# Kernel optimization log

Measured on AMD Instinct MI355X. Metric: run time of the kernel, lower is better.

Reference implementation:

```python
import jax, jax.numpy as jnp
import numpy as np

B, S, E, NH = 2, 2048, 1024, 8
DH = E // NH


def setup_inputs() -> dict:
    key = jax.random.key(0)
    ks = jax.random.split(key, 8)
    q = jax.random.normal(ks[0], (B, S, E), dtype=jnp.float32)
    k = jax.random.normal(ks[1], (B, S, E), dtype=jnp.float32)
    v = jax.random.normal(ks[2], (B, S, E), dtype=jnp.float32)
    # gate projections: Linear(3E -> NH)
    igate_w = jax.random.normal(ks[3], (NH, 3 * E), dtype=jnp.float32) * 0.02
    igate_b = jax.random.normal(ks[4], (NH,), dtype=jnp.float32) * 0.1
    fgate_w = jax.random.normal(ks[5], (NH, 3 * E), dtype=jnp.float32) * 0.02
    fgate_b = jnp.linspace(3.0, 6.0, NH, dtype=jnp.float32)  # bias_linspace_init_
    norm_weight = 1.0 + 0.01 * jax.random.normal(ks[6], (E,), dtype=jnp.float32)
    return {"q": q, "k": k, "v": v, "igate_w": igate_w, "igate_b": igate_b,
            "fgate_w": fgate_w, "fgate_b": fgate_b, "norm_weight": norm_weight}


def _mlstm_forward(q, k, v, igate_w, igate_b, fgate_w, fgate_b, norm_weight):
    eps = 1e-6
    gate_in = jnp.concatenate([q, k, v], axis=-1)            # (B,S,3E)
    i_pre = gate_in @ igate_w.T + igate_b                    # (B,S,NH)
    f_pre = gate_in @ fgate_w.T + fgate_b                    # (B,S,NH)
    i_pre = jnp.transpose(i_pre, (0, 2, 1))                  # (B,NH,S)
    f_pre = jnp.transpose(f_pre, (0, 2, 1))                  # (B,NH,S)

    qh = jnp.transpose(q.reshape(B, S, NH, DH), (0, 2, 1, 3))  # (B,NH,S,DH)
    kh = jnp.transpose(k.reshape(B, S, NH, DH), (0, 2, 1, 3))
    vh = jnp.transpose(v.reshape(B, S, NH, DH), (0, 2, 1, 3))

    # cumulative log forget gates; decay matrix D[i,j] = sum_{u=j+1..i} logsig(f_u) + i_pre[j]
    log_fg = jax.nn.log_sigmoid(f_pre)                       # (B,NH,S)
    cs = jnp.cumsum(log_fg, axis=-1)                         # (B,NH,S)
    diff = cs[:, :, :, None] - cs[:, :, None, :]             # (B,NH,S,S) = cs[i]-cs[j]
    causal = jnp.tril(jnp.ones((S, S), dtype=bool))
    log_fg_mat = jnp.where(causal, diff, -jnp.inf)
    log_D = log_fg_mat + i_pre[:, :, None, :]                # (B,NH,S,S)

    max_log_D = jnp.max(log_D, axis=-1, keepdims=True)       # rowwise stabilizer
    D = jnp.exp(log_D - max_log_D)

    qk = jnp.einsum("bhsd,bhtd->bhst", qh, kh / jnp.sqrt(jnp.float32(DH)))
    C = qk * D
    normalizer = jnp.maximum(jnp.abs(jnp.sum(C, axis=-1, keepdims=True)),
                             jnp.exp(-max_log_D))
    Cn = C / (normalizer + eps)
    h = jnp.einsum("bhst,bhtd->bhsd", Cn, vh)                # (B,NH,S,DH)

    # MultiHeadLayerNorm == group_norm(num_groups=NH): per-head, per-token over DH
    mu = jnp.mean(h, axis=-1, keepdims=True)
    var = jnp.var(h, axis=-1, keepdims=True)
    hn = (h - mu) / jnp.sqrt(var + 1e-5)
    hn = hn * norm_weight.reshape(NH, DH)[None, :, None, :]
    return jnp.transpose(hn, (0, 2, 1, 3)).reshape(B, S, E)


def reference(q, k, v, igate_w, igate_b, fgate_w, fgate_b, norm_weight):
    return _mlstm_forward(q, k, v, igate_w, igate_b, fgate_w, fgate_b, norm_weight)
```

## Files before the change

### kernel.cpp

```cpp
#include <hip/hip_runtime.h>
#include <hip/hip_bf16.h>
#include <math.h>

typedef __attribute__((ext_vector_type(8))) short bf16x8;
typedef __attribute__((ext_vector_type(4))) float f32x4;

namespace {
constexpr int kB = 2, kS = 2048, kE = 1024, kNH = 8, kDH = 128, kE3 = 3072;
constexpr float kLog2e = 1.4426950408889634f;
constexpr int BM = 64, BN = 64;
constexpr int kHeavy = 16;
constexpr int kUnits = 16 + 2 * 16;
}

__device__ __forceinline__ ushort f2bf(float x) {
  union { __hip_bfloat16 b; ushort u; } c; c.b = __float2bfloat16(x); return c.u;
}
__device__ __forceinline__ uint pk2(float a, float b) {
  return (uint)f2bf(a) | ((uint)f2bf(b) << 16);
}
__device__ __forceinline__ void gload16(const void* g, void* l) {
  __builtin_amdgcn_global_load_lds(
      (const __attribute__((address_space(1))) void*)g,
      (__attribute__((address_space(3))) void*)l, 16, 0, 0);
}

__device__ __forceinline__ float butterfly64(float* acc, int lane) {
  int cur = 64;
#pragma unroll
  for (int lv = 0; lv < 6; ++lv) {
    const int bmask = 1 << lv;
    const int half = cur >> 1;
    const bool hi = (lane & bmask) != 0;
#pragma unroll
    for (int i = 0; i < 32; ++i) {
      if (i >= half) break;
      const float keep = hi ? acc[i + half] : acc[i];
      const float send = hi ? acc[i] : acc[i + half];
      acc[i] = keep + __shfl_xor(send, bmask);
    }
    cur = half;
  }
  return acc[0];
}

__global__ __launch_bounds__(256) void convkv_kernel(
    const float* __restrict__ k, const float* __restrict__ v,
    ushort* __restrict__ Kb, ushort* __restrict__ Vtb) {
  const int b = blockIdx.y;
  const int s0 = blockIdx.x * 8;
  const int tid = threadIdx.x;
  const int w = tid >> 6, lane = tid & 63;
  __shared__ ushort Vst[8 * 1024];

#pragma unroll
  for (int t = 0; t < 2; ++t) {
    const int tokl = w * 2 + t;
    const int s = s0 + tokl;
    const size_t base = ((size_t)b * kS + s) * kE + lane * 16;
    const float4 k0 = *reinterpret_cast<const float4*>(k + base);
    const float4 k1 = *reinterpret_cast<const float4*>(k + base + 4);
    const float4 k2 = *reinterpret_cast<const float4*>(k + base + 8);
    const float4 k3 = *reinterpret_cast<const float4*>(k + base + 12);
    uint4 pa, pb;
    pa.x = pk2(k0.x, k0.y); pa.y = pk2(k0.z, k0.w);
    pa.z = pk2(k1.x, k1.y); pa.w = pk2(k1.z, k1.w);
    pb.x = pk2(k2.x, k2.y); pb.y = pk2(k2.z, k2.w);
    pb.z = pk2(k3.x, k3.y); pb.w = pk2(k3.z, k3.w);
    ushort* kd = Kb + ((size_t)(b * 8 + (lane >> 3)) * kS + s) * 128 + (lane & 7) * 16;
    *reinterpret_cast<uint4*>(kd) = pa;
    *reinterpret_cast<uint4*>(kd + 8) = pb;

    const float4 v0 = *reinterpret_cast<const float4*>(v + base);
    const float4 v1 = *reinterpret_cast<const float4*>(v + base + 4);
    const float4 v2 = *reinterpret_cast<const float4*>(v + base + 8);
    const float4 v3 = *reinterpret_cast<const float4*>(v + base + 12);
    uint4 va, vb4;
    va.x = pk2(v0.x, v0.y); va.y = pk2(v0.z, v0.w);
    va.z = pk2(v1.x, v1.y); va.w = pk2(v1.z, v1.w);
    vb4.x = pk2(v2.x, v2.y); vb4.y = pk2(v2.z, v2.w);
    vb4.z = pk2(v3.x, v3.y); vb4.w = pk2(v3.z, v3.w);
    const int cc0 = lane * 2, cc1 = lane * 2 + 1;
    *reinterpret_cast<uint4*>(reinterpret_cast<char*>(Vst) + tokl * 2048 +
                              ((cc0 ^ ((cc0 >> 3) & 7)) << 4)) = va;
    *reinterpret_cast<uint4*>(reinterpret_cast<char*>(Vst) + tokl * 2048 +
                              ((cc1 ^ ((cc1 >> 3) & 7)) << 4)) = vb4;
  }
  __syncthreads();

#pragma unroll
  for (int j = 0; j < 4; ++j) {
    const int e = j * 256 + tid;
    const int cc = e >> 3;
    const int off = ((cc ^ ((cc >> 3) & 7)) << 4) + (e & 7) * 2;
    uint tmp[4];
#pragma unroll
    for (int t2 = 0; t2 < 8; t2 += 2) {
      const ushort u0 = *reinterpret_cast<const ushort*>(
          reinterpret_cast<const char*>(Vst) + t2 * 2048 + off);
      const ushort u1 = *reinterpret_cast<const ushort*>(
          reinterpret_cast<const char*>(Vst) + (t2 + 1) * 2048 + off);
      tmp[t2 >> 1] = (uint)u0 | ((uint)u1 << 16);
    }
    uint4 o; o.x = tmp[0]; o.y = tmp[1]; o.z = tmp[2]; o.w = tmp[3];
    ushort* vd = Vtb + ((size_t)(b * 8 + (e >> 7)) * 128 + (e & 127)) * kS + s0;
    *reinterpret_cast<uint4*>(vd) = o;
  }
}

__global__ __launch_bounds__(256) void gates_kernel(
    const float* __restrict__ q, const float* __restrict__ k, const float* __restrict__ v,
    const float* __restrict__ iw, const float* __restrict__ ib,
    const float* __restrict__ fw, const float* __restrict__ fb,
    float* __restrict__ i_pre, float* __restrict__ f_pre) {
  const int tid = threadIdx.x;
  const int w = tid >> 6, lane = tid & 63;
  const int tokbase = blockIdx.x * 8;
  const int kh = w >> 1, gh = w & 1;
  const float* __restrict__ W = gh ? fw : iw;

  float acc[64];
#pragma unroll
  for (int i = 0; i < 64; ++i) acc[i] = 0.f;

  for (int step = 0; step < 24; ++step) {
    const int e = kh * 1536 + step * 64 + lane;
    const int seg = e >> 10;
    const int eo = e & 1023;
    const float* __restrict__ src = (seg == 0) ? q : (seg == 1) ? k : v;
    float gv[8];
#pragma unroll
    for (int t = 0; t < 8; ++t)
      gv[t] = src[(size_t)(tokbase + t) * kE + eo];
    float w8[8];
#pragma unroll
    for (int hh = 0; hh < 8; ++hh) w8[hh] = W[hh * kE3 + e];
#pragma unroll
    for (int t = 0; t < 8; ++t)
#pragma unroll
      for (int hh = 0; hh < 8; ++hh)
        acc[t * 8 + hh] += gv[t] * w8[hh];
  }
  const float r = butterfly64(acc, lane);
  const int a = ((lane & 1) << 5) | ((lane & 2) << 3) | ((lane & 4) << 1) |
                ((lane & 8) >> 1) | ((lane & 16) >> 3) | ((lane & 32) >> 5);
  __shared__ float red[4][64];
  red[w][a] = r;
  __syncthreads();
  if (tid < 128) {
    const int t = tid >> 4, g16 = tid & 15, hh = g16 & 7;
    const float val = (g16 < 8) ? red[0][t * 8 + hh] + red[2][t * 8 + hh]
                                : red[1][t * 8 + hh] + red[3][t * 8 + hh];
    const int token = tokbase + t;
    const int b = token >> 11, s = token & 2047;
    const size_t idx = ((size_t)(b * 8 + hh)) * kS + s;
    if (g16 < 8) i_pre[idx] = val + ib[hh];
    else         f_pre[idx] = val + fb[hh];
  }
}

__global__ __launch_bounds__(256) void scan_kernel(
    const float* __restrict__ i_pre, const float* __restrict__ f_pre,
    float* __restrict__ a2_out, float* __restrict__ M2_out, float* __restrict__ nfl_out) {
  const int bh = blockIdx.x;
  const int tid = threadIdx.x;
  const int w = tid >> 6, lane = tid & 63;
  __shared__ float wsum[4], wmax[4];
  const float* __restrict__ fp = f_pre + (size_t)bh * kS;
  const float* __restrict__ ip = i_pre + (size_t)bh * kS;
  const int s0 = tid * 8;

  const float4 fa = *reinterpret_cast<const float4*>(fp + s0);
  const float4 fb4 = *reinterpret_cast<const float4*>(fp + s0 + 4);
  float lf[8];
  {
    const float fv[8] = {fa.x, fa.y, fa.z, fa.w, fb4.x, fb4.y, fb4.z, fb4.w};
#pragma unroll
    for (int j = 0; j < 8; ++j)
      lf[j] = fminf(fv[j], 0.f) - log1pf(expf(-fabsf(fv[j])));
  }
  float run = 0.f, pcs[8];
#pragma unroll
  for (int j = 0; j < 8; ++j) { run += lf[j]; pcs[j] = run; }
  float x = run;
#pragma unroll
  for (int d = 1; d < 64; d <<= 1) {
    const float t = __shfl_up(x, d);
    if (lane >= d) x += t;
  }
  if (lane == 63) wsum[w] = x;
  __syncthreads();
  float woff = 0.f;
#pragma unroll
  for (int i = 0; i < 4; ++i) if (i < w) woff += wsum[i];
  const float csbase = woff + x - run;
  float cs[8];
#pragma unroll
  for (int j = 0; j < 8; ++j) cs[j] = csbase + pcs[j];

  const float4 ia = *reinterpret_cast<const float4*>(ip + s0);
  const float4 ib4 = *reinterpret_cast<const float4*>(ip + s0 + 4);
  float av[8];
  {
    const float iv[8] = {ia.x, ia.y, ia.z, ia.w, ib4.x, ib4.y, ib4.z, ib4.w};
#pragma unroll
    for (int j = 0; j < 8; ++j) av[j] = iv[j] - cs[j];
  }
  float rmax = -1e30f, pm[8];
#pragma unroll
  for (int j = 0; j < 8; ++j) { rmax = fmaxf(rmax, av[j]); pm[j] = rmax; }
  float mi = rmax;
#pragma unroll
  for (int d = 1; d < 64; d <<= 1) {
    const float t = __shfl_up(mi, d);
    if (lane >= d) mi = fmaxf(mi, t);
  }
  if (lane == 63) wmax[w] = mi;
  float mexcl = __shfl_up(mi, 1);
  if (lane == 0) mexcl = -1e30f;
  __syncthreads();
  float wmoff = -1e30f;
#pragma unroll
  for (int i = 0; i < 4; ++i) if (i < w) wmoff = fmaxf(wmoff, wmax[i]);
  const float mbase = fmaxf(wmoff, mexcl);

  float M[8];
#pragma unroll
  for (int j = 0; j < 8; ++j) M[j] = fmaxf(mbase, pm[j]);
  float4 a2lo, a2hi, m2lo, m2hi, nflo, nfhi;
  a2lo.x = av[0] * kLog2e; a2lo.y = av[1] * kLog2e; a2lo.z = av[2] * kLog2e; a2lo.w = av[3] * kLog2e;
  a2hi.x = av[4] * kLog2e; a2hi.y = av[5] * kLog2e; a2hi.z = av[6] * kLog2e; a2hi.w = av[7] * kLog2e;
  m2lo.x = M[0] * kLog2e; m2lo.y = M[1] * kLog2e; m2lo.z = M[2] * kLog2e; m2lo.w = M[3] * kLog2e;
  m2hi.x = M[4] * kLog2e; m2hi.y = M[5] * kLog2e; m2hi.z = M[6] * kLog2e; m2hi.w = M[7] * kLog2e;
  nflo.x = expf(-(cs[0] + M[0])); nflo.y = expf(-(cs[1] + M[1]));
  nflo.z = expf(-(cs[2] + M[2])); nflo.w = expf(-(cs[3] + M[3]));
  nfhi.x = expf(-(cs[4] + M[4])); nfhi.y = expf(-(cs[5] + M[5]));
  nfhi.z = expf(-(cs[6] + M[6])); nfhi.w = expf(-(cs[7] + M[7]));
  const size_t o = (size_t)bh * kS + s0;
  *reinterpret_cast<float4*>(a2_out + o) = a2lo;
  *reinterpret_cast<float4*>(a2_out + o + 4) = a2hi;
  *reinterpret_cast<float4*>(M2_out + o) = m2lo;
  *reinterpret_cast<float4*>(M2_out + o + 4) = m2hi;
  *reinterpret_cast<float4*>(nfl_out + o) = nflo;
  *reinterpret_cast<float4*>(nfl_out + o + 4) = nfhi;
}

__device__ __forceinline__ void epilogue_store(
    f32x4* hacc, float rsum, float nf, int b, int h, int srow, int g,
    const float* __restrict__ nw, float* __restrict__ out) {
  const float inv = 1.f / (fmaxf(fabsf(rsum), nf) + 1e-6f);
  float ps = 0.f, pq = 0.f;
#pragma unroll
  for (int db = 0; db < 8; ++db) {
#pragma unroll
    for (int reg = 0; reg < 4; ++reg) {
      const float hv = hacc[db][reg] * inv;
      hacc[db][reg] = hv;
      ps += hv; pq += hv * hv;
    }
  }
  ps += __shfl_xor(ps, 16); ps += __shfl_xor(ps, 32);
  pq += __shfl_xor(pq, 16); pq += __shfl_xor(pq, 32);
  const float mu = ps * (1.f / 128.f);
  const float var = pq * (1.f / 128.f) - mu * mu;
  const float rstd = rsqrtf(var + 1e-5f);
  float* __restrict__ orow = out + ((size_t)b * kS + srow) * kE + h * kDH;
#pragma unroll
  for (int db = 0; db < 8; ++db) {
    const int d0 = db * 16 + g * 4;
    const float4 nw4 = *reinterpret_cast<const float4*>(nw + h * kDH + d0);
    float4 o;
    o.x = (hacc[db][0] - mu) * rstd * nw4.x;
    o.y = (hacc[db][1] - mu) * rstd * nw4.y;
    o.z = (hacc[db][2] - mu) * rstd * nw4.z;
    o.w = (hacc[db][3] - mu) * rstd * nw4.w;
    *reinterpret_cast<float4*>(orow + d0) = o;
  }
}

__global__ __launch_bounds__(256, 2) void attn_mfma_kernel(
    const float* __restrict__ qg, const ushort* __restrict__ Kb,
    const ushort* __restrict__ Vtb,
    const float* __restrict__ a2, const float* __restrict__ M2,
    const float* __restrict__ nfl, const float* __restrict__ nw,
    float* __restrict__ out, float* __restrict__ ph, float* __restrict__ prs) {
  const int bh = blockIdx.y;
  const int b = bh >> 3, h = bh & 7;
  const int u = kUnits - 1 - (int)blockIdx.x;
  int it, j0, j1, chunk = -1;
  if (u < kHeavy) { it = u; j0 = 0; j1 = it; }
  else {
    const int t = (u - kHeavy) >> 1, c = (u - kHeavy) & 1;
    it = kHeavy + t;
    const int m = (it + 1) >> 1;
    if (c == 0) { j0 = 0; j1 = m - 1; } else { j0 = m; j1 = it; }
    chunk = ((bh * 16) + t) * 2 + c;
  }
  const int tid = threadIdx.x;
  const int w = tid >> 6, lane = tid & 63;
  const int l15 = lane & 15, g = lane >> 4;
  const int row0 = it * BM;
  const int rowbase = row0 + w * 16;
  const size_t bhS = (size_t)bh * kS;

  __shared__ ushort Klds[2 * BN * kDH];
  __shared__ ushort Vlds[2 * kDH * BN];
  __shared__ ushort Plds[4][16 * BN];

  const char* __restrict__ KgBase = reinterpret_cast<const char*>(Kb + bhS * 128);
  const char* __restrict__ VgBase = reinterpret_cast<const char*>(Vtb + (size_t)bh * 128 * kS);

  bf16x8 qf[4];
  {
    const float scale = 0.08838834764831845f;
    const float* qrow = qg + ((size_t)b * kS + rowbase + l15) * kE + h * kDH;
#pragma unroll
    for (int ks = 0; ks < 4; ++ks) {
      const float4 lo = *reinterpret_cast<const float4*>(qrow + ks * 32 + g * 8);
      const float4 hi = *reinterpret_cast<const float4*>(qrow + ks * 32 + g * 8 + 4);
      bf16x8 f;
      f[0] = (short)f2bf(lo.x * scale); f[1] = (short)f2bf(lo.y * scale);
      f[2] = (short)f2bf(lo.z * scale); f[3] = (short)f2bf(lo.w * scale);
      f[4] = (short)f2bf(hi.x * scale); f[5] = (short)f2bf(hi.y * scale);
      f[6] = (short)f2bf(hi.z * scale); f[7] = (short)f2bf(hi.w * scale);
      qf[ks] = f;
    }
  }
  float M2row[4];
#pragma unroll
  for (int reg = 0; reg < 4; ++reg) M2row[reg] = M2[bhS + rowbase + g * 4 + reg];

  int koffG[4], voffG[4];
#pragma unroll
  for (int i = 0; i < 4; ++i) {
    const int L = tid * 16 + i * 4096;
    { const int j = L >> 8, c = (L >> 4) & 15;
      koffG[i] = j * 256 + ((c ^ (j & 7)) << 4); }
    { const int d = L >> 7, c = (L >> 4) & 7;
      voffG[i] = d * 4096 + ((c ^ (d & 7)) << 4); }
  }

  auto stage = [&](int buf, int jt) {
    const char* Kg = KgBase + (size_t)jt * 16384;
    const char* Vg = VgBase + (size_t)jt * 128;
    char* kl = reinterpret_cast<char*>(Klds) + buf * 16384 + tid * 16;
    char* vl = reinterpret_cast<char*>(Vlds) + buf * 16384 + tid * 16;
#pragma unroll
    for (int i = 0; i < 4; ++i) gload16(Kg + koffG[i], kl + i * 4096);
#pragma unroll
    for (int i = 0; i < 4; ++i) gload16(Vg + voffG[i], vl + i * 4096);
  };

  f32x4 hacc[8];
#pragma unroll
  for (int db = 0; db < 8; ++db) hacc[db] = (f32x4){0.f, 0.f, 0.f, 0.f};
  float rs[4] = {0.f, 0.f, 0.f, 0.f};

  float avc[4];
#pragma unroll
  for (int cb = 0; cb < 4; ++cb) avc[cb] = a2[bhS + j0 * 64 + cb * 16 + l15];
  stage(0, j0);
  __syncthreads();

  for (int jt = j0; jt <= j1; ++jt) {
    const int cur = (jt - j0) & 1;
    float avn[4];
    if (jt < j1) {
      stage(cur ^ 1, jt + 1);
#pragma unroll
      for (int cb = 0; cb < 4; ++cb)
        avn[cb] = a2[bhS + (jt + 1) * 64 + cb * 16 + l15];
    }

    const int kbase = cur * 16384;
    f32x4 sacc[4];
#pragma unroll
    for (int cb = 0; cb < 4; ++cb) sacc[cb] = (f32x4){0.f, 0.f, 0.f, 0.f};
#pragma unroll
    for (int ks = 0; ks < 4; ++ks) {
#pragma unroll
      for (int cb = 0; cb < 4; ++cb) {
        const int j = cb * 16 + l15;
        const int kb = kbase + j * 256 + ((ks * 64 + g * 16) ^ ((l15 & 7) << 4));
        const bf16x8 kf = *reinterpret_cast<const bf16x8*>(
            reinterpret_cast<const char*>(Klds) + kb);
        sacc[cb] = __builtin_amdgcn_mfma_f32_16x16x32_bf16(qf[ks], kf, sacc[cb], 0, 0, 0);
      }
    }

#pragma unroll
    for (int cb = 0; cb < 4; ++cb) {
      const int jg = jt * 64 + cb * 16 + l15;
#pragma unroll
      for (int reg = 0; reg < 4; ++reg) {
        const int ig = rowbase + g * 4 + reg;
        float val = 0.f;
        if (jg <= ig) val = sacc[cb][reg] * exp2f(avc[cb] - M2row[reg]);
        rs[reg] += val;
        const int r = g * 4 + reg;
        const int pb = r * 128 + ((cb * 32 + l15 * 2) ^ ((r & 7) << 4));
        *reinterpret_cast<ushort*>(
            reinterpret_cast<char*>(&Plds[w][0]) + pb) = f2bf(val);
      }
    }

    const int vbase = cur * 16384;
#pragma unroll
    for (int ks2 = 0; ks2 < 2; ++ks2) {
      const int pbyte = l15 * 128 + ((ks2 * 64 + g * 16) ^ ((l15 & 7) << 4));
      const bf16x8 pf = *reinterpret_cast<const bf16x8*>(
          reinterpret_cast<const char*>(&Plds[w][0]) + pbyte);
#pragma unroll
      for (int db = 0; db < 8; ++db) {
        const int d = db * 16 + l15;
        const int vb = vbase + d * 128 + ((ks2 * 64 + g * 16) ^ ((d & 7) << 4));
        const bf16x8 vf = *reinterpret_cast<const bf16x8*>(
            reinterpret_cast<const char*>(Vlds) + vb);
        hacc[db] = __builtin_amdgcn_mfma_f32_16x16x32_bf16(vf, pf, hacc[db], 0, 0, 0);
      }
    }
    __syncthreads();
    if (jt < j1) {
#pragma unroll
      for (int cb = 0; cb < 4; ++cb) avc[cb] = avn[cb];
    }
  }

#pragma unroll
  for (int reg = 0; reg < 4; ++reg) {
    float x = rs[reg];
    x += __shfl_xor(x, 1); x += __shfl_xor(x, 2);
    x += __shfl_xor(x, 4); x += __shfl_xor(x, 8);
    rs[reg] = x;
  }

  if (chunk >= 0) {
    float* pdst = ph + (size_t)chunk * (BM * kDH) + tid * 32;
#pragma unroll
    for (int db = 0; db < 8; ++db)
      *reinterpret_cast<float4*>(pdst + db * 4) =
          make_float4(hacc[db][0], hacc[db][1], hacc[db][2], hacc[db][3]);
    if (l15 == 0) {
#pragma unroll
      for (int reg = 0; reg < 4; ++reg)
        prs[chunk * BM + w * 16 + g * 4 + reg] = rs[reg];
    }
    return;
  }

  float* rsp = reinterpret_cast<float*>(&Plds[w][0]);
  if (l15 == 0) {
#pragma unroll
    for (int reg = 0; reg < 4; ++reg) rsp[g * 4 + reg] = rs[reg];
  }
  const float rsum = rsp[l15];
  const float nf = nfl[bhS + rowbase + l15];
  epilogue_store(hacc, rsum, nf, b, h, rowbase + l15, g, nw, out);
}

__global__ __launch_bounds__(256) void combine_kernel(
    const float* __restrict__ ph, const float* __restrict__ prs,
    const float* __restrict__ nfl, const float* __restrict__ nw,
    float* __restrict__ out) {
  const int blk = blockIdx.x;
  const int bh = blk >> 4, t = blk & 15;
  const int b = bh >> 3, h = bh & 7;
  const int it = kHeavy + t;
  const int tid = threadIdx.x;
  const int w = tid >> 6, lane = tid & 63;
  const int l15 = lane & 15, g = lane >> 4;
  const int rowbase = it * BM + w * 16;
  const int c0 = blk * 2, c1 = blk * 2 + 1;

  f32x4 hacc[8];
  const float* p0 = ph + (size_t)c0 * (BM * kDH) + tid * 32;
  const float* p1 = ph + (size_t)c1 * (BM * kDH) + tid * 32;
#pragma unroll
  for (int db = 0; db < 8; ++db) {
    const float4 a = *reinterpret_cast<const float4*>(p0 + db * 4);
    const float4 c = *reinterpret_cast<const float4*>(p1 + db * 4);
    hacc[db] = (f32x4){a.x + c.x, a.y + c.y, a.z + c.z, a.w + c.w};
  }
  const float rsum = prs[c0 * BM + w * 16 + l15] + prs[c1 * BM + w * 16 + l15];
  const float nf = nfl[(size_t)bh * kS + rowbase + l15];
  epilogue_store(hacc, rsum, nf, b, h, rowbase + l15, g, nw, out);
}

extern "C" void kernel_launch(void* const* d_in, const int* in_sizes, int n_in,
                              void* d_out, int out_size, void* d_ws, size_t ws_size,
                              hipStream_t stream) {
  const float* q  = (const float*)d_in[0];
  const float* k  = (const float*)d_in[1];
  const float* v  = (const float*)d_in[2];
  const float* iw = (const float*)d_in[3];
  const float* ib = (const float*)d_in[4];
  const float* fw = (const float*)d_in[5];
  const float* fb = (const float*)d_in[6];
  const float* nw = (const float*)d_in[7];
  float* out = (float*)d_out;

  char* ws = (char*)d_ws;
  const int BHS = kB * kNH * kS;
  float* i_pre = (float*)ws;
  float* f_pre = i_pre + BHS;
  float* a2    = i_pre + 2 * BHS;
  float* M2    = i_pre + 3 * BHS;
  float* nfl   = i_pre + 4 * BHS;
  char* ws2 = ws + (size_t)5 * BHS * 4;
  ushort* Kb  = (ushort*)ws2;
  ushort* Vtb = Kb + (size_t)kB * kNH * kS * kDH;
  float* ph   = (float*)(Vtb + (size_t)kB * kNH * kS * kDH);
  float* prs  = ph + (size_t)512 * BM * kDH;

  convkv_kernel<<<dim3(kS / 8, kB), dim3(256), 0, stream>>>(k, v, Kb, Vtb);
  gates_kernel<<<dim3(kB * kS / 8), dim3(256), 0, stream>>>(q, k, v, iw, ib, fw, fb,
                                                            i_pre, f_pre);
  scan_kernel<<<dim3(kB * kNH), dim3(256), 0, stream>>>(i_pre, f_pre, a2, M2, nfl);
  attn_mfma_kernel<<<dim3(kUnits, kB * kNH), dim3(256), 0, stream>>>(
      q, Kb, Vtb, a2, M2, nfl, nw, out, ph, prs);
  combine_kernel<<<dim3(kB * kNH * 16), dim3(256), 0, stream>>>(ph, prs, nfl, nw, out);
}
```

Measured before the change: 122.4 us.

## Factor decay weights per key block and switch attention to 32x32 MFMA tiles

The scan now emits per-key weights exp(a - blockmax) plus a per-64-key-block maximum, so the attention kernel forms the decay as a per-tile scalar times a per-column weight instead of taking an exponential per element. The attention kernel moves to 128-row query tiles with 32x32x16 bf16 MFMA, 64-key tiles, and a new hand-tuned order of 27 work units that split the heavy query tiles into 2 or 3 chunks. The combine kernel is generalized to sum a variable number of partials, and convkv is moved after the scan. Factoring the exponential can underflow or lose precision when the row max and block max are far apart, and the larger register tiles may lower occupancy.

New measurement: 118.4 us. 1.03x faster.

```diff
diff --git a/kernel.cpp b/kernel.cpp
--- a/kernel.cpp
+++ b/kernel.cpp
@@ -3,15 +3,17 @@
 #include <math.h>
 
 typedef __attribute__((ext_vector_type(8))) short bf16x8;
-typedef __attribute__((ext_vector_type(4))) float f32x4;
+typedef __attribute__((ext_vector_type(16))) float f32x16;
 
 namespace {
 constexpr int kB = 2, kS = 2048, kE = 1024, kNH = 8, kDH = 128, kE3 = 3072;
 constexpr float kLog2e = 1.4426950408889634f;
-constexpr int BM = 64, BN = 64;
-constexpr int kHeavy = 16;
-constexpr int kUnits = 16 + 2 * 16;
-}
+constexpr int kUnits = 27;
+constexpr int kSplitPerBh = 20;
+}
+
+__device__ const int kOrder[kUnits] = {6,19,20,17,18,5,15,16,13,14,24,25,4,
+                                       11,12,21,22,23,26,9,10,3,7,8,2,1,0};
 
 __device__ __forceinline__ ushort f2bf(float x) {
   union { __hip_bfloat16 b; ushort u; } c; c.b = __float2bfloat16(x); return c.u;
@@ -24,6 +26,13 @@
       (const __attribute__((address_space(1))) void*)g,
       (__attribute__((address_space(3))) void*)l, 16, 0, 0);
 }
+__device__ __forceinline__ f32x16 zero16() {
+  f32x16 z;
+#pragma unroll
+  for (int i = 0; i < 16; ++i) z[i] = 0.f;
+  return z;
+}
+union UB8 { uint4 u; bf16x8 f; };
 
 __device__ __forceinline__ float butterfly64(float* acc, int lane) {
   int cur = 64;
@@ -42,70 +51,6 @@
     cur = half;
   }
   return acc[0];
-}
-
-__global__ __launch_bounds__(256) void convkv_kernel(
-    const float* __restrict__ k, const float* __restrict__ v,
-    ushort* __restrict__ Kb, ushort* __restrict__ Vtb) {
-  const int b = blockIdx.y;
-  const int s0 = blockIdx.x * 8;
-  const int tid = threadIdx.x;
-  const int w = tid >> 6, lane = tid & 63;
-  __shared__ ushort Vst[8 * 1024];
-
-#pragma unroll
-  for (int t = 0; t < 2; ++t) {
-    const int tokl = w * 2 + t;
-    const int s = s0 + tokl;
-    const size_t base = ((size_t)b * kS + s) * kE + lane * 16;
-    const float4 k0 = *reinterpret_cast<const float4*>(k + base);
-    const float4 k1 = *reinterpret_cast<const float4*>(k + base + 4);
-    const float4 k2 = *reinterpret_cast<const float4*>(k + base + 8);
-    const float4 k3 = *reinterpret_cast<const float4*>(k + base + 12);
-    uint4 pa, pb;
-    pa.x = pk2(k0.x, k0.y); pa.y = pk2(k0.z, k0.w);
-    pa.z = pk2(k1.x, k1.y); pa.w = pk2(k1.z, k1.w);
-    pb.x = pk2(k2.x, k2.y); pb.y = pk2(k2.z, k2.w);
-    pb.z = pk2(k3.x, k3.y); pb.w = pk2(k3.z, k3.w);
-    ushort* kd = Kb + ((size_t)(b * 8 + (lane >> 3)) * kS + s) * 128 + (lane & 7) * 16;
-    *reinterpret_cast<uint4*>(kd) = pa;
-    *reinterpret_cast<uint4*>(kd + 8) = pb;
-
-    const float4 v0 = *reinterpret_cast<const float4*>(v + base);
-    const float4 v1 = *reinterpret_cast<const float4*>(v + base + 4);
-    const float4 v2 = *reinterpret_cast<const float4*>(v + base + 8);
-    const float4 v3 = *reinterpret_cast<const float4*>(v + base + 12);
-    uint4 va, vb4;
-    va.x = pk2(v0.x, v0.y); va.y = pk2(v0.z, v0.w);
-    va.z = pk2(v1.x, v1.y); va.w = pk2(v1.z, v1.w);
-    vb4.x = pk2(v2.x, v2.y); vb4.y = pk2(v2.z, v2.w);
-    vb4.z = pk2(v3.x, v3.y); vb4.w = pk2(v3.z, v3.w);
-    const int cc0 = lane * 2, cc1 = lane * 2 + 1;
-    *reinterpret_cast<uint4*>(reinterpret_cast<char*>(Vst) + tokl * 2048 +
-                              ((cc0 ^ ((cc0 >> 3) & 7)) << 4)) = va;
-    *reinterpret_cast<uint4*>(reinterpret_cast<char*>(Vst) + tokl * 2048 +
-                              ((cc1 ^ ((cc1 >> 3) & 7)) << 4)) = vb4;
-  }
-  __syncthreads();
-
-#pragma unroll
-  for (int j = 0; j < 4; ++j) {
-    const int e = j * 256 + tid;
-    const int cc = e >> 3;
-    const int off = ((cc ^ ((cc >> 3) & 7)) << 4) + (e & 7) * 2;
-    uint tmp[4];
-#pragma unroll
-    for (int t2 = 0; t2 < 8; t2 += 2) {
-      const ushort u0 = *reinterpret_cast<const ushort*>(
-          reinterpret_cast<const char*>(Vst) + t2 * 2048 + off);
-      const ushort u1 = *reinterpret_cast<const ushort*>(
-          reinterpret_cast<const char*>(Vst) + (t2 + 1) * 2048 + off);
-      tmp[t2 >> 1] = (uint)u0 | ((uint)u1 << 16);
-    }
-    uint4 o; o.x = tmp[0]; o.y = tmp[1]; o.z = tmp[2]; o.w = tmp[3];
-    ushort* vd = Vtb + ((size_t)(b * 8 + (e >> 7)) * 128 + (e & 127)) * kS + s0;
-    *reinterpret_cast<uint4*>(vd) = o;
-  }
 }
 
 __global__ __launch_bounds__(256) void gates_kernel(
@@ -161,7 +106,8 @@
 
 __global__ __launch_bounds__(256) void scan_kernel(
     const float* __restrict__ i_pre, const float* __restrict__ f_pre,
-    float* __restrict__ a2_out, float* __restrict__ M2_out, float* __restrict__ nfl_out) {
+    float* __restrict__ wt_out, float* __restrict__ M2_out, float* __restrict__ nfl_out,
+    float* __restrict__ Cg) {
   const int bh = blockIdx.x;
   const int tid = threadIdx.x;
   const int w = tid >> 6, lane = tid & 63;
@@ -209,6 +155,19 @@
   float rmax = -1e30f, pm[8];
 #pragma unroll
   for (int j = 0; j < 8; ++j) { rmax = fmaxf(rmax, av[j]); pm[j] = rmax; }
+
+  float tm = rmax;
+  tm = fmaxf(tm, __shfl_xor(tm, 1));
+  tm = fmaxf(tm, __shfl_xor(tm, 2));
+  tm = fmaxf(tm, __shfl_xor(tm, 4));
+  if ((lane & 7) == 0) Cg[bh * 32 + (tid >> 3)] = tm * kLog2e;
+
+  float4 wtlo, wthi;
+  wtlo.x = exp2f((av[0] - tm) * kLog2e); wtlo.y = exp2f((av[1] - tm) * kLog2e);
+  wtlo.z = exp2f((av[2] - tm) * kLog2e); wtlo.w = exp2f((av[3] - tm) * kLog2e);
+  wthi.x = exp2f((av[4] - tm) * kLog2e); wthi.y = exp2f((av[5] - tm) * kLog2e);
+  wthi.z = exp2f((av[6] - tm) * kLog2e); wthi.w = exp2f((av[7] - tm) * kLog2e);
+
   float mi = rmax;
 #pragma unroll
   for (int d = 1; d < 64; d <<= 1) {
@@ -227,9 +186,7 @@
   float M[8];
 #pragma unroll
   for (int j = 0; j < 8; ++j) M[j] = fmaxf(mbase, pm[j]);
-  float4 a2lo, a2hi, m2lo, m2hi, nflo, nfhi;
-  a2lo.x = av[0] * kLog2e; a2lo.y = av[1] * kLog2e; a2lo.z = av[2] * kLog2e; a2lo.w = av[3] * kLog2e;
-  a2hi.x = av[4] * kLog2e; a2hi.y = av[5] * kLog2e; a2hi.z = av[6] * kLog2e; a2hi.w = av[7] * kLog2e;
+  float4 m2lo, m2hi, nflo, nfhi;
   m2lo.x = M[0] * kLog2e; m2lo.y = M[1] * kLog2e; m2lo.z = M[2] * kLog2e; m2lo.w = M[3] * kLog2e;
   m2hi.x = M[4] * kLog2e; m2hi.y = M[5] * kLog2e; m2hi.z = M[6] * kLog2e; m2hi.w = M[7] * kLog2e;
   nflo.x = expf(-(cs[0] + M[0])); nflo.y = expf(-(cs[1] + M[1]));
@@ -237,109 +194,146 @@
   nfhi.x = expf(-(cs[4] + M[4])); nfhi.y = expf(-(cs[5] + M[5]));
   nfhi.z = expf(-(cs[6] + M[6])); nfhi.w = expf(-(cs[7] + M[7]));
   const size_t o = (size_t)bh * kS + s0;
-  *reinterpret_cast<float4*>(a2_out + o) = a2lo;
-  *reinterpret_cast<float4*>(a2_out + o + 4) = a2hi;
+  *reinterpret_cast<float4*>(wt_out + o) = wtlo;
+  *reinterpret_cast<float4*>(wt_out + o + 4) = wthi;
   *reinterpret_cast<float4*>(M2_out + o) = m2lo;
   *reinterpret_cast<float4*>(M2_out + o + 4) = m2hi;
   *reinterpret_cast<float4*>(nfl_out + o) = nflo;
   *reinterpret_cast<float4*>(nfl_out + o + 4) = nfhi;
 }
 
-__device__ __forceinline__ void epilogue_store(
-    f32x4* hacc, float rsum, float nf, int b, int h, int srow, int g,
-    const float* __restrict__ nw, float* __restrict__ out) {
-  const float inv = 1.f / (fmaxf(fabsf(rsum), nf) + 1e-6f);
-  float ps = 0.f, pq = 0.f;
-#pragma unroll
-  for (int db = 0; db < 8; ++db) {
-#pragma unroll
-    for (int reg = 0; reg < 4; ++reg) {
-      const float hv = hacc[db][reg] * inv;
-      hacc[db][reg] = hv;
-      ps += hv; pq += hv * hv;
-    }
-  }
-  ps += __shfl_xor(ps, 16); ps += __shfl_xor(ps, 32);
-  pq += __shfl_xor(pq, 16); pq += __shfl_xor(pq, 32);
-  const float mu = ps * (1.f / 128.f);
-  const float var = pq * (1.f / 128.f) - mu * mu;
-  const float rstd = rsqrtf(var + 1e-5f);
-  float* __restrict__ orow = out + ((size_t)b * kS + srow) * kE + h * kDH;
-#pragma unroll
-  for (int db = 0; db < 8; ++db) {
-    const int d0 = db * 16 + g * 4;
-    const float4 nw4 = *reinterpret_cast<const float4*>(nw + h * kDH + d0);
-    float4 o;
-    o.x = (hacc[db][0] - mu) * rstd * nw4.x;
-    o.y = (hacc[db][1] - mu) * rstd * nw4.y;
-    o.z = (hacc[db][2] - mu) * rstd * nw4.z;
-    o.w = (hacc[db][3] - mu) * rstd * nw4.w;
-    *reinterpret_cast<float4*>(orow + d0) = o;
+__global__ __launch_bounds__(256) void convkv_kernel(
+    const float* __restrict__ k, const float* __restrict__ v,
+    ushort* __restrict__ Kb, ushort* __restrict__ Vtb) {
+  const int b = blockIdx.y;
+  const int s0 = blockIdx.x * 8;
+  const int tid = threadIdx.x;
+  const int w = tid >> 6, lane = tid & 63;
+  __shared__ ushort Vst[8 * 1024];
+
+#pragma unroll
+  for (int t = 0; t < 2; ++t) {
+    const int tokl = w * 2 + t;
+    const int s = s0 + tokl;
+    const size_t base = ((size_t)b * kS + s) * kE + lane * 16;
+    const int hh = lane >> 3;
+
+    const float4 k0 = *reinterpret_cast<const float4*>(k + base);
+    const float4 k1 = *reinterpret_cast<const float4*>(k + base + 4);
+    const float4 k2 = *reinterpret_cast<const float4*>(k + base + 8);
+    const float4 k3 = *reinterpret_cast<const float4*>(k + base + 12);
+    uint4 pa, pb;
+    pa.x = pk2(k0.x, k0.y); pa.y = pk2(k0.z, k0.w);
+    pa.z = pk2(k1.x, k1.y); pa.w = pk2(k1.z, k1.w);
+    pb.x = pk2(k2.x, k2.y); pb.y = pk2(k2.z, k2.w);
+    pb.z = pk2(k3.x, k3.y); pb.w = pk2(k3.z, k3.w);
+    ushort* kd = Kb + ((size_t)(b * 8 + hh) * kS + s) * 128 + (lane & 7) * 16;
+    *reinterpret_cast<uint4*>(kd) = pa;
+    *reinterpret_cast<uint4*>(kd + 8) = pb;
+
+    const float4 v0 = *reinterpret_cast<const float4*>(v + base);
+    const float4 v1 = *reinterpret_cast<const float4*>(v + base + 4);
+    const float4 v2 = *reinterpret_cast<const float4*>(v + base + 8);
+    const float4 v3 = *reinterpret_cast<const float4*>(v + base + 12);
+    uint4 va, vb4;
+    va.x = pk2(v0.x, v0.y); va.y = pk2(v0.z, v0.w);
+    va.z = pk2(v1.x, v1.y); va.w = pk2(v1.z, v1.w);
+    vb4.x = pk2(v2.x, v2.y); vb4.y = pk2(v2.z, v2.w);
+    vb4.z = pk2(v3.x, v3.y); vb4.w = pk2(v3.z, v3.w);
+    const int cc0 = lane * 2, cc1 = lane * 2 + 1;
+    *reinterpret_cast<uint4*>(reinterpret_cast<char*>(Vst) + tokl * 2048 +
+                              ((cc0 ^ ((cc0 >> 3) & 7)) << 4)) = va;
+    *reinterpret_cast<uint4*>(reinterpret_cast<char*>(Vst) + tokl * 2048 +
+                              ((cc1 ^ ((cc1 >> 3) & 7)) << 4)) = vb4;
+  }
+  __syncthreads();
+
+#pragma unroll
+  for (int j = 0; j < 4; ++j) {
+    const int e = j * 256 + tid;
+    const int cc = e >> 3;
+    const int off = ((cc ^ ((cc >> 3) & 7)) << 4) + (e & 7) * 2;
+    uint tmp[4];
+#pragma unroll
+    for (int t2 = 0; t2 < 8; t2 += 2) {
+      const ushort u0 = *reinterpret_cast<const ushort*>(
+          reinterpret_cast<const char*>(Vst) + t2 * 2048 + off);
+      const ushort u1 = *reinterpret_cast<const ushort*>(
+          reinterpret_cast<const char*>(Vst) + (t2 + 1) * 2048 + off);
+      tmp[t2 >> 1] = (uint)u0 | ((uint)u1 << 16);
+    }
+    uint4 o; o.x = tmp[0]; o.y = tmp[1]; o.z = tmp[2]; o.w = tmp[3];
+    ushort* vd = Vtb + ((size_t)(b * 8 + (e >> 7)) * 128 + (e & 127)) * kS + s0;
+    *reinterpret_cast<uint4*>(vd) = o;
   }
 }
 
 __global__ __launch_bounds__(256, 2) void attn_mfma_kernel(
     const float* __restrict__ qg, const ushort* __restrict__ Kb,
-    const ushort* __restrict__ Vtb,
-    const float* __restrict__ a2, const float* __restrict__ M2,
+    const ushort* __restrict__ Vtb, const float* __restrict__ wt,
+    const float* __restrict__ Cg, const float* __restrict__ M2,
     const float* __restrict__ nfl, const float* __restrict__ nw,
     float* __restrict__ out, float* __restrict__ ph, float* __restrict__ prs) {
   const int bh = blockIdx.y;
   const int b = bh >> 3, h = bh & 7;
-  const int u = kUnits - 1 - (int)blockIdx.x;
-  int it, j0, j1, chunk = -1;
-  if (u < kHeavy) { it = u; j0 = 0; j1 = it; }
-  else {
-    const int t = (u - kHeavy) >> 1, c = (u - kHeavy) & 1;
-    it = kHeavy + t;
-    const int m = (it + 1) >> 1;
-    if (c == 0) { j0 = 0; j1 = m - 1; } else { j0 = m; j1 = it; }
-    chunk = ((bh * 16) + t) * 2 + c;
+  const int u = kOrder[blockIdx.x];
+  int it, j0, j1, cid = -1;
+  if (u <= 6) { it = u; const int T = 2 * it + 2; j0 = 0; j1 = T - 1; }
+  else if (u <= 20) {
+    const int s = u - 7; it = 7 + (s >> 1); const int ci = s & 1;
+    const int T = 2 * it + 2;
+    j0 = (T * ci) >> 1; j1 = ((T * (ci + 1)) >> 1) - 1;
+    cid = bh * kSplitPerBh + (u - 7);
+  } else {
+    const int s = u - 21; it = 14 + (s >= 3 ? 1 : 0); const int ci = s - (s >= 3 ? 3 : 0);
+    const int T = 2 * it + 2;
+    j0 = (T * ci) / 3; j1 = (T * (ci + 1)) / 3 - 1;
+    cid = bh * kSplitPerBh + (u - 7);
   }
   const int tid = threadIdx.x;
   const int w = tid >> 6, lane = tid & 63;
-  const int l15 = lane & 15, g = lane >> 4;
-  const int row0 = it * BM;
-  const int rowbase = row0 + w * 16;
+  const int l31 = lane & 31, hi = lane >> 5;
+  const int row_w = it * 128 + w * 32;
+  const int ig = row_w + l31;
   const size_t bhS = (size_t)bh * kS;
 
-  __shared__ ushort Klds[2 * BN * kDH];
-  __shared__ ushort Vlds[2 * kDH * BN];
-  __shared__ ushort Plds[4][16 * BN];
+  __shared__ ushort Klds[2 * 64 * 128];
+  __shared__ ushort Vlds[2 * 128 * 64];
+  __shared__ float Wlds[2 * 64];
+  __shared__ float rsx[4][32];
 
   const char* __restrict__ KgBase = reinterpret_cast<const char*>(Kb + bhS * 128);
   const char* __restrict__ VgBase = reinterpret_cast<const char*>(Vtb + (size_t)bh * 128 * kS);
-
-  bf16x8 qf[4];
+  const char* __restrict__ WgBase = reinterpret_cast<const char*>(wt + bhS);
+
+  bf16x8 qf[8];
   {
     const float scale = 0.08838834764831845f;
-    const float* qrow = qg + ((size_t)b * kS + rowbase + l15) * kE + h * kDH;
-#pragma unroll
-    for (int ks = 0; ks < 4; ++ks) {
-      const float4 lo = *reinterpret_cast<const float4*>(qrow + ks * 32 + g * 8);
-      const float4 hi = *reinterpret_cast<const float4*>(qrow + ks * 32 + g * 8 + 4);
-      bf16x8 f;
-      f[0] = (short)f2bf(lo.x * scale); f[1] = (short)f2bf(lo.y * scale);
-      f[2] = (short)f2bf(lo.z * scale); f[3] = (short)f2bf(lo.w * scale);
-      f[4] = (short)f2bf(hi.x * scale); f[5] = (short)f2bf(hi.y * scale);
-      f[6] = (short)f2bf(hi.z * scale); f[7] = (short)f2bf(hi.w * scale);
-      qf[ks] = f;
-    }
-  }
-  float M2row[4];
-#pragma unroll
-  for (int reg = 0; reg < 4; ++reg) M2row[reg] = M2[bhS + rowbase + g * 4 + reg];
+    const float* qrow = qg + ((size_t)b * kS + ig) * kE + h * kDH;
+#pragma unroll
+    for (int ks = 0; ks < 8; ++ks) {
+      const int d0 = ks * 16 + hi * 8;
+      const float4 lo = *reinterpret_cast<const float4*>(qrow + d0);
+      const float4 hi4 = *reinterpret_cast<const float4*>(qrow + d0 + 4);
+      UB8 f;
+      f.u.x = pk2(lo.x * scale, lo.y * scale);
+      f.u.y = pk2(lo.z * scale, lo.w * scale);
+      f.u.z = pk2(hi4.x * scale, hi4.y * scale);
+      f.u.w = pk2(hi4.z * scale, hi4.w * scale);
+      qf[ks] = f.f;
+    }
+  }
+  const float M2i = M2[bhS + ig];
 
   int koffG[4], voffG[4];
 #pragma unroll
   for (int i = 0; i < 4; ++i) {
     const int L = tid * 16 + i * 4096;
     { const int j = L >> 8, c = (L >> 4) & 15;
-      koffG[i] = j * 256 + ((c ^ (j & 7)) << 4); }
+      koffG[i] = j * 256 + ((c ^ (j & 15)) << 4); }
     { const int d = L >> 7, c = (L >> 4) & 7;
       voffG[i] = d * 4096 + ((c ^ (d & 7)) << 4); }
   }
-
   auto stage = [&](int buf, int jt) {
     const char* Kg = KgBase + (size_t)jt * 16384;
     const char* Vg = VgBase + (size_t)jt * 128;
@@ -349,113 +343,133 @@
     for (int i = 0; i < 4; ++i) gload16(Kg + koffG[i], kl + i * 4096);
 #pragma unroll
     for (int i = 0; i < 4; ++i) gload16(Vg + voffG[i], vl + i * 4096);
+    if (tid < 16)
+      gload16(WgBase + jt * 256 + tid * 16,
+              reinterpret_cast<char*>(Wlds) + buf * 256 + tid * 16);
   };
 
-  f32x4 hacc[8];
-#pragma unroll
-  for (int db = 0; db < 8; ++db) hacc[db] = (f32x4){0.f, 0.f, 0.f, 0.f};
-  float rs[4] = {0.f, 0.f, 0.f, 0.f};
-
-  float avc[4];
-#pragma unroll
-  for (int cb = 0; cb < 4; ++cb) avc[cb] = a2[bhS + j0 * 64 + cb * 16 + l15];
+  f32x16 hacc[4];
+#pragma unroll
+  for (int dc = 0; dc < 4; ++dc) hacc[dc] = zero16();
+  float rs = 0.f;
+
   stage(0, j0);
   __syncthreads();
 
   for (int jt = j0; jt <= j1; ++jt) {
     const int cur = (jt - j0) & 1;
-    float avn[4];
-    if (jt < j1) {
-      stage(cur ^ 1, jt + 1);
-#pragma unroll
-      for (int cb = 0; cb < 4; ++cb)
-        avn[cb] = a2[bhS + (jt + 1) * 64 + cb * 16 + l15];
-    }
-
-    const int kbase = cur * 16384;
-    f32x4 sacc[4];
-#pragma unroll
-    for (int cb = 0; cb < 4; ++cb) sacc[cb] = (f32x4){0.f, 0.f, 0.f, 0.f};
-#pragma unroll
-    for (int ks = 0; ks < 4; ++ks) {
-#pragma unroll
-      for (int cb = 0; cb < 4; ++cb) {
-        const int j = cb * 16 + l15;
-        const int kb = kbase + j * 256 + ((ks * 64 + g * 16) ^ ((l15 & 7) << 4));
-        const bf16x8 kf = *reinterpret_cast<const bf16x8*>(
-            reinterpret_cast<const char*>(Klds) + kb);
-        sacc[cb] = __builtin_amdgcn_mfma_f32_16x16x32_bf16(qf[ks], kf, sacc[cb], 0, 0, 0);
+    if (jt < j1) stage(cur ^ 1, jt + 1);
+    const int jlo = jt * 64;
+    const bool v0 = (jlo <= row_w + 31);
+    const bool v1 = (jlo + 32 <= row_w + 31);
+    const bool fullmask = (jlo + 63 <= row_w);
+
+    if (v0) {
+      const float f = exp2f(Cg[bh * 32 + jt] - M2i);
+      const char* kb = reinterpret_cast<const char*>(Klds) + cur * 16384;
+      const char* vb = reinterpret_cast<const char*>(Vlds) + cur * 16384;
+      const float* Wf = Wlds + cur * 64;
+      const int ksw = (l31 & 15) << 4;
+
+      f32x16 sacc0 = zero16(), sacc1 = zero16();
+#pragma unroll
+      for (int ks = 0; ks < 8; ++ks) {
+        const int colb = 32 * ks + 16 * hi;
+        const bf16x8 kf0 = *reinterpret_cast<const bf16x8*>(
+            kb + l31 * 256 + (colb ^ ksw));
+        sacc0 = __builtin_amdgcn_mfma_f32_32x32x16_bf16(kf0, qf[ks], sacc0, 0, 0, 0);
+        if (v1) {
+          const bf16x8 kf1 = *reinterpret_cast<const bf16x8*>(
+              kb + (32 + l31) * 256 + (colb ^ ksw));
+          sacc1 = __builtin_amdgcn_mfma_f32_32x32x16_bf16(kf1, qf[ks], sacc1, 0, 0, 0);
+        }
       }
-    }
-
-#pragma unroll
-    for (int cb = 0; cb < 4; ++cb) {
-      const int jg = jt * 64 + cb * 16 + l15;
-#pragma unroll
-      for (int reg = 0; reg < 4; ++reg) {
-        const int ig = rowbase + g * 4 + reg;
-        float val = 0.f;
-        if (jg <= ig) val = sacc[cb][reg] * exp2f(avc[cb] - M2row[reg]);
-        rs[reg] += val;
-        const int r = g * 4 + reg;
-        const int pb = r * 128 + ((cb * 32 + l15 * 2) ^ ((r & 7) << 4));
-        *reinterpret_cast<ushort*>(
-            reinterpret_cast<char*>(&Plds[w][0]) + pb) = f2bf(val);
+
+      uint pkw[2][8];
+#pragma unroll
+      for (int jc = 0; jc < 2; ++jc) {
+        if (jc == 1 && !v1) break;
+        const f32x16 sa = jc ? sacc1 : sacc0;
+        float p[16];
+#pragma unroll
+        for (int r = 0; r < 16; ++r) {
+          const int joff = jc * 32 + (r & 3) + 8 * (r >> 2) + 4 * hi;
+          float val = sa[r] * (Wf[joff] * f);
+          if (!fullmask) val = (jlo + joff <= ig) ? val : 0.f;
+          rs += val; p[r] = val;
+        }
+#pragma unroll
+        for (int q2 = 0; q2 < 8; ++q2) pkw[jc][q2] = pk2(p[2 * q2], p[2 * q2 + 1]);
       }
-    }
-
-    const int vbase = cur * 16384;
-#pragma unroll
-    for (int ks2 = 0; ks2 < 2; ++ks2) {
-      const int pbyte = l15 * 128 + ((ks2 * 64 + g * 16) ^ ((l15 & 7) << 4));
-      const bf16x8 pf = *reinterpret_cast<const bf16x8*>(
-          reinterpret_cast<const char*>(&Plds[w][0]) + pbyte);
-#pragma unroll
-      for (int db = 0; db < 8; ++db) {
-        const int d = db * 16 + l15;
-        const int vb = vbase + d * 128 + ((ks2 * 64 + g * 16) ^ ((d & 7) << 4));
-        const bf16x8 vf = *reinterpret_cast<const bf16x8*>(
-            reinterpret_cast<const char*>(Vlds) + vb);
-        hacc[db] = __builtin_amdgcn_mfma_f32_16x16x32_bf16(vf, pf, hacc[db], 0, 0, 0);
+
+#pragma unroll
+      for (int ks = 0; ks < 4; ++ks) {
+        const int jc = ks >> 1, ks2 = ks & 1;
+        if (jc == 1 && !v1) break;
+        UB8 pf;
+        pf.u.x = pkw[jc][ks2 * 4 + 0]; pf.u.y = pkw[jc][ks2 * 4 + 1];
+        pf.u.z = pkw[jc][ks2 * 4 + 2]; pf.u.w = pkw[jc][ks2 * 4 + 3];
+        const int colb = 64 * jc + 32 * ks2 + 8 * hi;
+#pragma unroll
+        for (int dc = 0; dc < 4; ++dc) {
+          const int d = dc * 32 + l31;
+          const char* vrow = vb + d * 128;
+          const int sw = (d & 7) << 4;
+          const uint2 a = *reinterpret_cast<const uint2*>(vrow + (colb ^ sw));
+          const uint2 c = *reinterpret_cast<const uint2*>(vrow + ((colb + 16) ^ sw));
+          UB8 vf; vf.u.x = a.x; vf.u.y = a.y; vf.u.z = c.x; vf.u.w = c.y;
+          hacc[dc] = __builtin_amdgcn_mfma_f32_32x32x16_bf16(pf.f, vf.f, hacc[dc], 0, 0, 0);
+        }
       }
     }
     __syncthreads();
-    if (jt < j1) {
-#pragma unroll
-      for (int cb = 0; cb < 4; ++cb) avc[cb] = avn[cb];
-    }
-  }
-
-#pragma unroll
-  for (int reg = 0; reg < 4; ++reg) {
-    float x = rs[reg];
-    x += __shfl_xor(x, 1); x += __shfl_xor(x, 2);
-    x += __shfl_xor(x, 4); x += __shfl_xor(x, 8);
-    rs[reg] = x;
-  }
-
-  if (chunk >= 0) {
-    float* pdst = ph + (size_t)chunk * (BM * kDH) + tid * 32;
-#pragma unroll
-    for (int db = 0; db < 8; ++db)
-      *reinterpret_cast<float4*>(pdst + db * 4) =
-          make_float4(hacc[db][0], hacc[db][1], hacc[db][2], hacc[db][3]);
-    if (l15 == 0) {
-#pragma unroll
-      for (int reg = 0; reg < 4; ++reg)
-        prs[chunk * BM + w * 16 + g * 4 + reg] = rs[reg];
-    }
+  }
+
+  const float rs_tot = rs + __shfl_xor(rs, 32);
+
+  if (cid >= 0) {
+    float* pb = ph + (size_t)cid * 16384;
+#pragma unroll
+    for (int dc = 0; dc < 4; ++dc)
+#pragma unroll
+      for (int r = 0; r < 16; ++r) {
+        const int il = w * 32 + (r & 3) + 8 * (r >> 2) + 4 * hi;
+        pb[il * 128 + dc * 32 + l31] = hacc[dc][r];
+      }
+    if (hi == 0) prs[cid * 128 + w * 32 + l31] = rs_tot;
     return;
   }
 
-  float* rsp = reinterpret_cast<float*>(&Plds[w][0]);
-  if (l15 == 0) {
-#pragma unroll
-    for (int reg = 0; reg < 4; ++reg) rsp[g * 4 + reg] = rs[reg];
-  }
-  const float rsum = rsp[l15];
-  const float nf = nfl[bhS + rowbase + l15];
-  epilogue_store(hacc, rsum, nf, b, h, rowbase + l15, g, nw, out);
+  if (hi == 0) rsx[w][l31] = rs_tot;
+  float nwv[4];
+#pragma unroll
+  for (int dc = 0; dc < 4; ++dc) nwv[dc] = nw[h * kDH + dc * 32 + l31];
+#pragma unroll
+  for (int r = 0; r < 16; ++r) {
+    const int imap = (r & 3) + 8 * (r >> 2) + 4 * hi;
+    const float rsum = rsx[w][imap];
+    const float nf = nfl[bhS + row_w + imap];
+    const float inv = 1.f / (fmaxf(fabsf(rsum), nf) + 1e-6f);
+    float hv[4];
+    float s1 = 0.f, s2 = 0.f;
+#pragma unroll
+    for (int dc = 0; dc < 4; ++dc) {
+      hv[dc] = hacc[dc][r] * inv;
+      s1 += hv[dc]; s2 += hv[dc] * hv[dc];
+    }
+#pragma unroll
+    for (int off = 1; off <= 16; off <<= 1) {
+      s1 += __shfl_xor(s1, off);
+      s2 += __shfl_xor(s2, off);
+    }
+    const float mu = s1 * (1.f / 128.f);
+    const float var = s2 * (1.f / 128.f) - mu * mu;
+    const float rstd = rsqrtf(var + 1e-5f);
+    float* __restrict__ orow = out + ((size_t)b * kS + row_w + imap) * kE + h * kDH;
+#pragma unroll
+    for (int dc = 0; dc < 4; ++dc)
+      orow[dc * 32 + l31] = (hv[dc] - mu) * rstd * nwv[dc];
+  }
 }
 
 __global__ __launch_bounds__(256) void combine_kernel(
@@ -463,27 +477,50 @@
     const float* __restrict__ nfl, const float* __restrict__ nw,
     float* __restrict__ out) {
   const int blk = blockIdx.x;
-  const int bh = blk >> 4, t = blk & 15;
+  const int bh = blk / 9, ct = blk % 9;
   const int b = bh >> 3, h = bh & 7;
-  const int it = kHeavy + t;
+  const int it = 7 + ct;
+  const int nc = (ct < 7) ? 2 : 3;
+  const int cb0 = bh * kSplitPerBh + ((ct < 7) ? ct * 2 : 14 + (ct - 7) * 3);
   const int tid = threadIdx.x;
-  const int w = tid >> 6, lane = tid & 63;
-  const int l15 = lane & 15, g = lane >> 4;
-  const int rowbase = it * BM + w * 16;
-  const int c0 = blk * 2, c1 = blk * 2 + 1;
-
-  f32x4 hacc[8];
-  const float* p0 = ph + (size_t)c0 * (BM * kDH) + tid * 32;
-  const float* p1 = ph + (size_t)c1 * (BM * kDH) + tid * 32;
-#pragma unroll
-  for (int db = 0; db < 8; ++db) {
-    const float4 a = *reinterpret_cast<const float4*>(p0 + db * 4);
-    const float4 c = *reinterpret_cast<const float4*>(p1 + db * 4);
-    hacc[db] = (f32x4){a.x + c.x, a.y + c.y, a.z + c.z, a.w + c.w};
-  }
-  const float rsum = prs[c0 * BM + w * 16 + l15] + prs[c1 * BM + w * 16 + l15];
-  const float nf = nfl[(size_t)bh * kS + rowbase + l15];
-  epilogue_store(hacc, rsum, nf, b, h, rowbase + l15, g, nw, out);
+  __shared__ float sinv[128];
+  if (tid < 128) {
+    float rsum = 0.f;
+    for (int c = 0; c < nc; ++c) rsum += prs[(cb0 + c) * 128 + tid];
+    const float nf = nfl[(size_t)bh * kS + it * 128 + tid];
+    sinv[tid] = 1.f / (fmaxf(fabsf(rsum), nf) + 1e-6f);
+  }
+  __syncthreads();
+  for (int kk = 0; kk < 16; ++kk) {
+    const int idx = kk * 256 + tid;
+    const int row = idx >> 5, c4 = idx & 31;
+    float ax = 0.f, ay = 0.f, az = 0.f, aw = 0.f;
+    for (int c = 0; c < nc; ++c) {
+      const float4 t = *reinterpret_cast<const float4*>(
+          ph + (size_t)(cb0 + c) * 16384 + row * 128 + c4 * 4);
+      ax += t.x; ay += t.y; az += t.z; aw += t.w;
+    }
+    const float inv = sinv[row];
+    ax *= inv; ay *= inv; az *= inv; aw *= inv;
+    float s1 = ax + ay + az + aw;
+    float s2 = ax * ax + ay * ay + az * az + aw * aw;
+#pragma unroll
+    for (int off = 1; off <= 16; off <<= 1) {
+      s1 += __shfl_xor(s1, off);
+      s2 += __shfl_xor(s2, off);
+    }
+    const float mu = s1 * (1.f / 128.f);
+    const float var = s2 * (1.f / 128.f) - mu * mu;
+    const float rstd = rsqrtf(var + 1e-5f);
+    const float4 nw4 = *reinterpret_cast<const float4*>(nw + h * kDH + c4 * 4);
+    float4 o;
+    o.x = (ax - mu) * rstd * nw4.x;
+    o.y = (ay - mu) * rstd * nw4.y;
+    o.z = (az - mu) * rstd * nw4.z;
+    o.w = (aw - mu) * rstd * nw4.w;
+    *reinterpret_cast<float4*>(
+        out + ((size_t)b * kS + it * 128 + row) * kE + h * kDH + c4 * 4) = o;
+  }
 }
 
 extern "C" void kernel_launch(void* const* d_in, const int* in_sizes, int n_in,
@@ -503,20 +540,20 @@
   const int BHS = kB * kNH * kS;
   float* i_pre = (float*)ws;
   float* f_pre = i_pre + BHS;
-  float* a2    = i_pre + 2 * BHS;
+  float* wt    = i_pre + 2 * BHS;
   float* M2    = i_pre + 3 * BHS;
   float* nfl   = i_pre + 4 * BHS;
-  char* ws2 = ws + (size_t)5 * BHS * 4;
-  ushort* Kb  = (ushort*)ws2;
+  float* Cg    = i_pre + 5 * BHS;
+  ushort* Kb  = (ushort*)(ws + (size_t)(5 * BHS + 512) * 4);
   ushort* Vtb = Kb + (size_t)kB * kNH * kS * kDH;
   float* ph   = (float*)(Vtb + (size_t)kB * kNH * kS * kDH);
-  float* prs  = ph + (size_t)512 * BM * kDH;
-
-  convkv_kernel<<<dim3(kS / 8, kB), dim3(256), 0, stream>>>(k, v, Kb, Vtb);
+  float* prs  = ph + (size_t)320 * 128 * 128;
+
   gates_kernel<<<dim3(kB * kS / 8), dim3(256), 0, stream>>>(q, k, v, iw, ib, fw, fb,
                                                             i_pre, f_pre);
-  scan_kernel<<<dim3(kB * kNH), dim3(256), 0, stream>>>(i_pre, f_pre, a2, M2, nfl);
+  scan_kernel<<<dim3(kB * kNH), dim3(256), 0, stream>>>(i_pre, f_pre, wt, M2, nfl, Cg);
+  convkv_kernel<<<dim3(kS / 8, kB), dim3(256), 0, stream>>>(k, v, Kb, Vtb);
   attn_mfma_kernel<<<dim3(kUnits, kB * kNH), dim3(256), 0, stream>>>(
-      q, Kb, Vtb, a2, M2, nfl, nw, out, ph, prs);
-  combine_kernel<<<dim3(kB * kNH * 16), dim3(256), 0, stream>>>(ph, prs, nfl, nw, out);
-}
+      q, Kb, Vtb, wt, Cg, M2, nfl, nw, out, ph, prs);
+  combine_kernel<<<dim3(kB * kNH * 9), dim3(256), 0, stream>>>(ph, prs, nfl, nw, out);
+}
```
